# Optimization experiments

Measured on AMD Instinct MI355X. Metric: run time of the kernel, lower is better.

## Reference

```python
import jax, jax.numpy as jnp
import numpy as np

N_NODES = 9
NEG_SLOPE = 0.2
# static edge list from the module (src, dst) pairs, PyG convention row0=src, row1=dst
_E = np.array([[0,1],[1,0],[0,3],[3,0],[0,5],[5,0],[0,7],[7,0],
               [1,2],[2,1],[3,4],[4,3],[5,6],[6,5],[7,8],[8,7]], dtype=np.int32).T
# GATv2Conv default add_self_loops=True
SRC = jnp.asarray(np.concatenate([_E[0], np.arange(N_NODES, dtype=np.int32)]))
DST = jnp.asarray(np.concatenate([_E[1], np.arange(N_NODES, dtype=np.int32)]))


def setup_inputs() -> dict:
    key = jax.random.key(0)
    k1, k2, k3, k4 = jax.random.split(key, 4)
    B, C_IN, C_OUT = 16384, 256, 256
    scale = 1.0 / np.sqrt(C_IN)
    return {
        "x": jax.random.normal(k1, (B, N_NODES, C_IN), jnp.float32),
        "W_l": jax.random.normal(k2, (C_IN, C_OUT), jnp.float32) * scale,
        "W_r": jax.random.normal(k3, (C_IN, C_OUT), jnp.float32) * scale,
        "att": jax.random.normal(k4, (C_OUT,), jnp.float32) * scale,
        "bias": jnp.zeros((C_OUT,), jnp.float32),
    }


def reference(x, W_l, W_r, att, bias):
    # x: [B, N, C_in] batch of identical small graphs
    xl = jnp.einsum("bnc,cd->bnd", x, W_l)  # source-side projection
    xr = jnp.einsum("bnc,cd->bnd", x, W_r)  # target-side projection
    # per-edge GATv2 score: a^T LeakyReLU(x_l[src] + x_r[dst])
    e = jax.nn.leaky_relu(xl[:, SRC] + xr[:, DST], NEG_SLOPE)  # [B, E, C_out]
    score = jnp.einsum("bed,d->be", e, att)                    # [B, E]
    # softmax over incoming edges of each destination node (segment softmax)
    sT = score.T                                               # [E, B]
    m = jax.ops.segment_max(sT, DST, num_segments=N_NODES)     # [N, B]
    ex = jnp.exp(sT - m[DST])
    denom = jax.ops.segment_sum(ex, DST, num_segments=N_NODES)
    alpha = ex / denom[DST]                                    # [E, B]
    # scatter-aggregate messages alpha * x_l[src] into dst
    msg = xl[:, SRC] * alpha.T[..., None]                      # [B, E, C_out]
    out = jax.ops.segment_sum(msg.transpose(1, 0, 2), DST, num_segments=N_NODES)
    return out.transpose(1, 0, 2) + bias                       # [B, N, C_out]
```

## Files before the change

kernel.cpp:

```cpp
#include <hip/hip_runtime.h>
#include <hip/hip_bf16.h>

typedef __attribute__((ext_vector_type(8))) short short8;
typedef __attribute__((ext_vector_type(4))) float f32x4;
typedef __attribute__((ext_vector_type(4))) unsigned short u16x4;

#define STAGE_BYTES (144 * 512)
#define PART_OFF    0
#define ALPHA_OFF   (8 * 25 * 16 * 4)
#define LDS_BYTES   STAGE_BYTES

__device__ __forceinline__ unsigned short f2bf(float f) {
    unsigned int u = __float_as_uint(f);
    unsigned int r = (u + 0x7fffu + ((u >> 16) & 1u)) >> 16;
    return (unsigned short)r;
}

constexpr int C_SRC[25] = {0,1,0,3,0,5,0,7,1,2,3,4,5,6,7,8, 0,1,2,3,4,5,6,7,8};
constexpr int C_DST[25] = {1,0,3,0,5,0,7,0,2,1,4,3,6,5,8,7, 0,1,2,3,4,5,6,7,8};
constexpr int C_NINC[9]  = {5,3,2,3,2,3,2,3,2};
constexpr int C_IOFF[9]  = {0,5,8,10,13,15,18,20,23};
constexpr int C_INCE[25] = {1,3,5,7,16, 0,9,17, 8,18, 2,11,19, 10,20, 4,13,21, 12,22, 6,15,23, 14,24};
constexpr int C_INCS[25] = {1,3,5,7,0,  0,2,1,  1,2,  0,4,3,  3,4,  0,6,5,  5,6,  0,8,7,  7,8};
__device__ const int D_NINC[9]  = {5,3,2,3,2,3,2,3,2};
__device__ const int D_IOFF[9]  = {0,5,8,10,13,15,18,20,23};
__device__ const int D_INCE[25] = {1,3,5,7,16, 0,9,17, 8,18, 2,11,19, 10,20, 4,13,21, 12,22, 6,15,23, 14,24};

__global__ void convert_w_kernel(const float* __restrict__ Wl,
                                 const float* __restrict__ Wr,
                                 unsigned short* __restrict__ WT) {
    int n = blockIdx.x;
    int k = threadIdx.x;
    float v = (n < 256) ? Wl[k * 256 + n] : Wr[k * 256 + (n - 256)];
    WT[n * 256 + k] = f2bf(v);
}

__global__ __launch_bounds__(512, 2) void gat_fused_kernel(
        const float* __restrict__ x,
        const unsigned short* __restrict__ WT,
        const float* __restrict__ att,
        const float* __restrict__ bias,
        float* __restrict__ out) {
    __shared__ __align__(16) char smem[LDS_BYTES];
    float* partials = (float*)(smem + PART_OFF);
    float* alphas   = (float*)(smem + ALPHA_OFF);

    const int tid  = threadIdx.x;
    const int lane = tid & 63;
    const int w    = tid >> 6;
    const int gl   = lane >> 4;
    const int li   = lane & 15;
    const int blk  = blockIdx.x;

    const int c0 = 32 * w + li, c1 = c0 + 16;
    const float attc0 = att[c0], attc1 = att[c1];
    const float bc0   = bias[c0], bc1 = bias[c1];

    const float* xblk = x + (size_t)blk * 36864;
    {
        f32x4 xv[18];
        #pragma unroll
        for (int it = 0; it < 18; ++it)
            xv[it] = *(const f32x4*)(xblk + it * 2048 + tid * 4);
        #pragma unroll
        for (int it = 0; it < 18; ++it) {
            int f    = it * 2048 + tid * 4;
            int gr   = f >> 8;
            int c    = f & 255;
            int g    = gr / 9;
            int node = gr - g * 9;
            int srow = node * 16 + g;
            u16x4 pk = { f2bf(xv[it][0]), f2bf(xv[it][1]), f2bf(xv[it][2]), f2bf(xv[it][3]) };
            *(u16x4*)(smem + srow * 512 + ((2 * c) ^ (g << 4))) = pk;
        }
    }
    __syncthreads();

    const f32x4 ZERO = {0.f, 0.f, 0.f, 0.f};
    f32x4 aL[9][2], aR[9][2];
    #pragma unroll
    for (int m = 0; m < 9; ++m) {
        aL[m][0] = ZERO; aL[m][1] = ZERO; aR[m][0] = ZERO; aR[m][1] = ZERO;
    }
    const unsigned short* WL0 = WT + (size_t)((32 * w + li) * 256 + gl * 8);
    const unsigned short* WL1 = WL0 + 16 * 256;
    const unsigned short* WR0 = WL0 + 256 * 256;
    const unsigned short* WR1 = WR0 + 16 * 256;

    #pragma unroll
    for (int kc = 0; kc < 8; ++kc) {
        short8 bl0 = *(const short8*)(WL0 + kc * 32);
        short8 bl1 = *(const short8*)(WL1 + kc * 32);
        short8 br0 = *(const short8*)(WR0 + kc * 32);
        short8 br1 = *(const short8*)(WR1 + kc * 32);
        const int inner = ((kc * 64) + (gl * 16)) ^ (li << 4);
        short8 am[9];
        #pragma unroll
        for (int m = 0; m < 9; ++m)
            am[m] = *(const short8*)(smem + (m * 16 + li) * 512 + inner);
        #pragma unroll
        for (int m = 0; m < 9; ++m) {
            aL[m][0] = __builtin_amdgcn_mfma_f32_16x16x32_bf16(am[m], bl0, aL[m][0], 0, 0, 0);
            aL[m][1] = __builtin_amdgcn_mfma_f32_16x16x32_bf16(am[m], bl1, aL[m][1], 0, 0, 0);
            aR[m][0] = __builtin_amdgcn_mfma_f32_16x16x32_bf16(am[m], br0, aR[m][0], 0, 0, 0);
            aR[m][1] = __builtin_amdgcn_mfma_f32_16x16x32_bf16(am[m], br1, aR[m][1], 0, 0, 0);
        }
    }
    __syncthreads();

    #pragma unroll
    for (int e = 0; e < 25; ++e) {
        const int s = C_SRC[e], d = C_DST[e];
        float p0 = 0.f, p1 = 0.f, p2 = 0.f, p3 = 0.f;
        #pragma unroll
        for (int nt = 0; nt < 2; ++nt) {
            const float ac = nt ? attc1 : attc0;
            #pragma unroll
            for (int r = 0; r < 4; ++r) {
                float v  = aL[s][nt][r] + aR[d][nt][r];
                float lr = fmaxf(v, 0.2f * v);
                float t  = ac * lr;
                if (r == 0) p0 += t; else if (r == 1) p1 += t;
                else if (r == 2) p2 += t; else p3 += t;
            }
        }
        #pragma unroll
        for (int m = 1; m < 16; m <<= 1) {
            p0 += __shfl_xor(p0, m);
            p1 += __shfl_xor(p1, m);
            p2 += __shfl_xor(p2, m);
            p3 += __shfl_xor(p3, m);
        }
        if (li == 0) {
            f32x4 pk = {p0, p1, p2, p3};
            *(f32x4*)(partials + (w * 25 + e) * 16 + 4 * gl) = pk;
        }
    }
    __syncthreads();

    if (tid < 144) {
        int n = tid >> 4, g = tid & 15;
        int off = D_IOFF[n], cnt = D_NINC[n];
        float mx = -1e30f;
        for (int i = 0; i < cnt; ++i) {
            int e = D_INCE[off + i];
            float s = 0.f;
            #pragma unroll
            for (int ww = 0; ww < 8; ++ww) s += partials[(ww * 25 + e) * 16 + g];
            alphas[e * 16 + g] = s;
            mx = fmaxf(mx, s);
        }
        float ssum = 0.f;
        for (int i = 0; i < cnt; ++i)
            ssum += __expf(alphas[D_INCE[off + i] * 16 + g] - mx);
        float inv = 1.f / ssum;
        for (int i = 0; i < cnt; ++i) {
            int e = D_INCE[off + i];
            alphas[e * 16 + g] = __expf(alphas[e * 16 + g] - mx) * inv;
        }
    }
    __syncthreads();

    #pragma unroll
    for (int n = 0; n < 9; ++n) {
        f32x4 o0 = {bc0, bc0, bc0, bc0};
        f32x4 o1 = {bc1, bc1, bc1, bc1};
        #pragma unroll
        for (int i = 0; i < C_NINC[n]; ++i) {
            const int e  = C_INCE[C_IOFF[n] + i];
            const int sn = C_INCS[C_IOFF[n] + i];
            f32x4 al = *(const f32x4*)(alphas + e * 16 + 4 * gl);
            #pragma unroll
            for (int r = 0; r < 4; ++r) {
                o0[r] += al[r] * aL[sn][0][r];
                o1[r] += al[r] * aL[sn][1][r];
            }
        }
        #pragma unroll
        for (int r = 0; r < 4; ++r) {
            size_t row = (size_t)(blk * 16 + 4 * gl + r) * 9 + n;
            out[row * 256 + c0] = o0[r];
            out[row * 256 + c1] = o1[r];
        }
    }
}

extern "C" void kernel_launch(void* const* d_in, const int* in_sizes, int n_in,
                              void* d_out, int out_size, void* d_ws, size_t ws_size,
                              hipStream_t stream) {
    const float* x    = (const float*)d_in[0];
    const float* Wl   = (const float*)d_in[1];
    const float* Wr   = (const float*)d_in[2];
    const float* att  = (const float*)d_in[3];
    const float* bias = (const float*)d_in[4];
    float* out = (float*)d_out;
    unsigned short* WT = (unsigned short*)d_ws;

    convert_w_kernel<<<512, 256, 0, stream>>>(Wl, Wr, WT);
    gat_fused_kernel<<<1024, 512, 0, stream>>>(x, WT, att, bias, out);
}
```

Before: 140.9 us.

## Split fused GAT block across 16 waves, one 16-column tile per wave

The fused kernel goes from 512 to 1024 threads per block, and each of the 16 waves now owns a single 16-column output tile instead of two. Per-thread accumulator registers drop by half and the staging loads drop from 18 to 9 per thread, aiming for more wavefronts resident per CU and better latency hiding. In exchange, every A fragment is read from LDS twice as often across waves, the cross-wave partial-score reduction doubles to 16 entries, and the launch bound of (1024,4) may force register limits or spills.

Result: slower. 175.9 us (+24.9%).

```diff
diff --git a/kernel.cpp b/kernel.cpp
--- a/kernel.cpp
+++ b/kernel.cpp
@@ -7,7 +7,7 @@
 
 #define STAGE_BYTES (144 * 512)
 #define PART_OFF    0
-#define ALPHA_OFF   (8 * 25 * 16 * 4)
+#define ALPHA_OFF   (16 * 25 * 16 * 4)
 #define LDS_BYTES   STAGE_BYTES
 
 __device__ __forceinline__ unsigned short f2bf(float f) {
@@ -35,7 +35,7 @@
     WT[n * 256 + k] = f2bf(v);
 }
 
-__global__ __launch_bounds__(512, 2) void gat_fused_kernel(
+__global__ __launch_bounds__(1024, 4) void gat_fused_kernel(
         const float* __restrict__ x,
         const unsigned short* __restrict__ WT,
         const float* __restrict__ att,
@@ -52,19 +52,19 @@
     const int li   = lane & 15;
     const int blk  = blockIdx.x;
 
-    const int c0 = 32 * w + li, c1 = c0 + 16;
-    const float attc0 = att[c0], attc1 = att[c1];
-    const float bc0   = bias[c0], bc1 = bias[c1];
+    const int c0 = 16 * w + li;
+    const float attc = att[c0];
+    const float bc   = bias[c0];
 
     const float* xblk = x + (size_t)blk * 36864;
     {
-        f32x4 xv[18];
+        f32x4 xv[9];
         #pragma unroll
-        for (int it = 0; it < 18; ++it)
-            xv[it] = *(const f32x4*)(xblk + it * 2048 + tid * 4);
+        for (int it = 0; it < 9; ++it)
+            xv[it] = *(const f32x4*)(xblk + it * 4096 + tid * 4);
         #pragma unroll
-        for (int it = 0; it < 18; ++it) {
-            int f    = it * 2048 + tid * 4;
+        for (int it = 0; it < 9; ++it) {
+            int f    = it * 4096 + tid * 4;
             int gr   = f >> 8;
             int c    = f & 255;
             int g    = gr / 9;
@@ -77,33 +77,23 @@
     __syncthreads();
 
     const f32x4 ZERO = {0.f, 0.f, 0.f, 0.f};
-    f32x4 aL[9][2], aR[9][2];
+    f32x4 aL[9], aR[9];
     #pragma unroll
-    for (int m = 0; m < 9; ++m) {
-        aL[m][0] = ZERO; aL[m][1] = ZERO; aR[m][0] = ZERO; aR[m][1] = ZERO;
-    }
-    const unsigned short* WL0 = WT + (size_t)((32 * w + li) * 256 + gl * 8);
-    const unsigned short* WL1 = WL0 + 16 * 256;
-    const unsigned short* WR0 = WL0 + 256 * 256;
-    const unsigned short* WR1 = WR0 + 16 * 256;
+    for (int m = 0; m < 9; ++m) { aL[m] = ZERO; aR[m] = ZERO; }
+
+    const unsigned short* WL = WT + (size_t)(c0 * 256 + gl * 8);
+    const unsigned short* WR = WL + 256 * 256;
 
     #pragma unroll
     for (int kc = 0; kc < 8; ++kc) {
-        short8 bl0 = *(const short8*)(WL0 + kc * 32);
-        short8 bl1 = *(const short8*)(WL1 + kc * 32);
-        short8 br0 = *(const short8*)(WR0 + kc * 32);
-        short8 br1 = *(const short8*)(WR1 + kc * 32);
+        short8 bl = *(const short8*)(WL + kc * 32);
+        short8 br = *(const short8*)(WR + kc * 32);
         const int inner = ((kc * 64) + (gl * 16)) ^ (li << 4);
-        short8 am[9];
-        #pragma unroll
-        for (int m = 0; m < 9; ++m)
-            am[m] = *(const short8*)(smem + (m * 16 + li) * 512 + inner);
         #pragma unroll
         for (int m = 0; m < 9; ++m) {
-            aL[m][0] = __builtin_amdgcn_mfma_f32_16x16x32_bf16(am[m], bl0, aL[m][0], 0, 0, 0);
-            aL[m][1] = __builtin_amdgcn_mfma_f32_16x16x32_bf16(am[m], bl1, aL[m][1], 0, 0, 0);
-            aR[m][0] = __builtin_amdgcn_mfma_f32_16x16x32_bf16(am[m], br0, aR[m][0], 0, 0, 0);
-            aR[m][1] = __builtin_amdgcn_mfma_f32_16x16x32_bf16(am[m], br1, aR[m][1], 0, 0, 0);
+            short8 a = *(const short8*)(smem + (m * 16 + li) * 512 + inner);
+            aL[m] = __builtin_amdgcn_mfma_f32_16x16x32_bf16(a, bl, aL[m], 0, 0, 0);
+            aR[m] = __builtin_amdgcn_mfma_f32_16x16x32_bf16(a, br, aR[m], 0, 0, 0);
         }
     }
     __syncthreads();
@@ -111,18 +101,16 @@
     #pragma unroll
     for (int e = 0; e < 25; ++e) {
         const int s = C_SRC[e], d = C_DST[e];
-        float p0 = 0.f, p1 = 0.f, p2 = 0.f, p3 = 0.f;
-        #pragma unroll
-        for (int nt = 0; nt < 2; ++nt) {
-            const float ac = nt ? attc1 : attc0;
-            #pragma unroll
-            for (int r = 0; r < 4; ++r) {
-                float v  = aL[s][nt][r] + aR[d][nt][r];
-                float lr = fmaxf(v, 0.2f * v);
-                float t  = ac * lr;
-                if (r == 0) p0 += t; else if (r == 1) p1 += t;
-                else if (r == 2) p2 += t; else p3 += t;
-            }
+        float p0, p1, p2, p3;
+        {
+            float v0 = aL[s][0] + aR[d][0];
+            float v1 = aL[s][1] + aR[d][1];
+            float v2 = aL[s][2] + aR[d][2];
+            float v3 = aL[s][3] + aR[d][3];
+            p0 = attc * fmaxf(v0, 0.2f * v0);
+            p1 = attc * fmaxf(v1, 0.2f * v1);
+            p2 = attc * fmaxf(v2, 0.2f * v2);
+            p3 = attc * fmaxf(v3, 0.2f * v3);
         }
         #pragma unroll
         for (int m = 1; m < 16; m <<= 1) {
@@ -146,7 +134,7 @@
             int e = D_INCE[off + i];
             float s = 0.f;
             #pragma unroll
-            for (int ww = 0; ww < 8; ++ww) s += partials[(ww * 25 + e) * 16 + g];
+            for (int ww = 0; ww < 16; ++ww) s += partials[(ww * 25 + e) * 16 + g];
             alphas[e * 16 + g] = s;
             mx = fmaxf(mx, s);
         }
@@ -163,24 +151,20 @@
 
     #pragma unroll
     for (int n = 0; n < 9; ++n) {
-        f32x4 o0 = {bc0, bc0, bc0, bc0};
-        f32x4 o1 = {bc1, bc1, bc1, bc1};
+        f32x4 o = {bc, bc, bc, bc};
         #pragma unroll
         for (int i = 0; i < C_NINC[n]; ++i) {
             const int e  = C_INCE[C_IOFF[n] + i];
             const int sn = C_INCS[C_IOFF[n] + i];
             f32x4 al = *(const f32x4*)(alphas + e * 16 + 4 * gl);
             #pragma unroll
-            for (int r = 0; r < 4; ++r) {
-                o0[r] += al[r] * aL[sn][0][r];
-                o1[r] += al[r] * aL[sn][1][r];
-            }
+            for (int r = 0; r < 4; ++r)
+                o[r] += al[r] * aL[sn][r];
         }
         #pragma unroll
         for (int r = 0; r < 4; ++r) {
             size_t row = (size_t)(blk * 16 + 4 * gl + r) * 9 + n;
-            out[row * 256 + c0] = o0[r];
-            out[row * 256 + c1] = o1[r];
+            out[row * 256 + c0] = o[r];
         }
     }
 }
@@ -197,5 +181,5 @@
     unsigned short* WT = (unsigned short*)d_ws;
 
     convert_w_kernel<<<512, 256, 0, stream>>>(Wl, Wr, WT);
-    gat_fused_kernel<<<1024, 512, 0, stream>>>(x, WT, att, bias, out);
+    gat_fused_kernel<<<1024, 1024, 0, stream>>>(x, WT, att, bias, out);
 }
```

## Pack projection accumulators to bf16 and split GEMM phases to raise occupancy

Applied to the files above, without the earlier changes.

The kernel now computes the right projection first and then the left projection in two halves over the node rows. Each finished fp32 accumulator is packed into bf16 pairs, so far fewer registers stay live. The launch bound goes from 2 to 4 blocks per SM, and the x staging loads are split into two batches to cut peak register use. The aim is higher occupancy to hide memory latency. The cost is rounding the xl/xr values to bf16 before the attention scores and the aggregation, which reduces accuracy, plus reloading W and LDS rows across the separate phases.

After: 554.8 us. 3.94x slower.

```diff
diff --git a/kernel.cpp b/kernel.cpp
--- a/kernel.cpp
+++ b/kernel.cpp
@@ -15,6 +15,8 @@
     unsigned int r = (u + 0x7fffu + ((u >> 16) & 1u)) >> 16;
     return (unsigned short)r;
 }
+__device__ __forceinline__ float bflo(unsigned int u) { return __uint_as_float(u << 16); }
+__device__ __forceinline__ float bfhi(unsigned int u) { return __uint_as_float(u & 0xffff0000u); }
 
 constexpr int C_SRC[25] = {0,1,0,3,0,5,0,7,1,2,3,4,5,6,7,8, 0,1,2,3,4,5,6,7,8};
 constexpr int C_DST[25] = {1,0,3,0,5,0,7,0,2,1,4,3,6,5,8,7, 0,1,2,3,4,5,6,7,8};
@@ -35,7 +37,7 @@
     WT[n * 256 + k] = f2bf(v);
 }
 
-__global__ __launch_bounds__(512, 2) void gat_fused_kernel(
+__global__ __launch_bounds__(512, 4) void gat_fused_kernel(
         const float* __restrict__ x,
         const unsigned short* __restrict__ WT,
         const float* __restrict__ att,
@@ -57,14 +59,15 @@
     const float bc0   = bias[c0], bc1 = bias[c1];
 
     const float* xblk = x + (size_t)blk * 36864;
-    {
-        f32x4 xv[18];
-        #pragma unroll
-        for (int it = 0; it < 18; ++it)
-            xv[it] = *(const f32x4*)(xblk + it * 2048 + tid * 4);
-        #pragma unroll
-        for (int it = 0; it < 18; ++it) {
-            int f    = it * 2048 + tid * 4;
+    #pragma unroll
+    for (int b = 0; b < 2; ++b) {
+        f32x4 xv[9];
+        #pragma unroll
+        for (int it = 0; it < 9; ++it)
+            xv[it] = *(const f32x4*)(xblk + (b * 9 + it) * 2048 + tid * 4);
+        #pragma unroll
+        for (int it = 0; it < 9; ++it) {
+            int f    = (b * 9 + it) * 2048 + tid * 4;
             int gr   = f >> 8;
             int c    = f & 255;
             int g    = gr / 9;
@@ -76,34 +79,68 @@
     }
     __syncthreads();
 
+    const unsigned short* WL = WT + (size_t)(c0 * 256 + gl * 8);
+    const unsigned short* WR = WL + 256 * 256;
     const f32x4 ZERO = {0.f, 0.f, 0.f, 0.f};
-    f32x4 aL[9][2], aR[9][2];
-    #pragma unroll
-    for (int m = 0; m < 9; ++m) {
-        aL[m][0] = ZERO; aL[m][1] = ZERO; aR[m][0] = ZERO; aR[m][1] = ZERO;
-    }
-    const unsigned short* WL0 = WT + (size_t)((32 * w + li) * 256 + gl * 8);
-    const unsigned short* WL1 = WL0 + 16 * 256;
-    const unsigned short* WR0 = WL0 + 256 * 256;
-    const unsigned short* WR1 = WR0 + 16 * 256;
-
-    #pragma unroll
-    for (int kc = 0; kc < 8; ++kc) {
-        short8 bl0 = *(const short8*)(WL0 + kc * 32);
-        short8 bl1 = *(const short8*)(WL1 + kc * 32);
-        short8 br0 = *(const short8*)(WR0 + kc * 32);
-        short8 br1 = *(const short8*)(WR1 + kc * 32);
-        const int inner = ((kc * 64) + (gl * 16)) ^ (li << 4);
-        short8 am[9];
+
+    unsigned int aRb[9][2][2];
+    unsigned int aLb[9][2][2];
+
+    {
+        f32x4 aR[9][2];
+        #pragma unroll
+        for (int m = 0; m < 9; ++m) { aR[m][0] = ZERO; aR[m][1] = ZERO; }
+        #pragma unroll
+        for (int kc = 0; kc < 8; ++kc) {
+            short8 br0 = *(const short8*)(WR + kc * 32);
+            short8 br1 = *(const short8*)(WR + 16 * 256 + kc * 32);
+            const int inner = ((kc * 64) + (gl * 16)) ^ (li << 4);
+            #pragma unroll
+            for (int m = 0; m < 9; ++m) {
+                short8 a = *(const short8*)(smem + (m * 16 + li) * 512 + inner);
+                aR[m][0] = __builtin_amdgcn_mfma_f32_16x16x32_bf16(a, br0, aR[m][0], 0, 0, 0);
+                aR[m][1] = __builtin_amdgcn_mfma_f32_16x16x32_bf16(a, br1, aR[m][1], 0, 0, 0);
+            }
+        }
         #pragma unroll
         for (int m = 0; m < 9; ++m)
-            am[m] = *(const short8*)(smem + (m * 16 + li) * 512 + inner);
-        #pragma unroll
-        for (int m = 0; m < 9; ++m) {
-            aL[m][0] = __builtin_amdgcn_mfma_f32_16x16x32_bf16(am[m], bl0, aL[m][0], 0, 0, 0);
-            aL[m][1] = __builtin_amdgcn_mfma_f32_16x16x32_bf16(am[m], bl1, aL[m][1], 0, 0, 0);
-            aR[m][0] = __builtin_amdgcn_mfma_f32_16x16x32_bf16(am[m], br0, aR[m][0], 0, 0, 0);
-            aR[m][1] = __builtin_amdgcn_mfma_f32_16x16x32_bf16(am[m], br1, aR[m][1], 0, 0, 0);
+            #pragma unroll
+            for (int nt = 0; nt < 2; ++nt) {
+                aRb[m][nt][0] = (unsigned int)f2bf(aR[m][nt][0]) | ((unsigned int)f2bf(aR[m][nt][1]) << 16);
+                aRb[m][nt][1] = (unsigned int)f2bf(aR[m][nt][2]) | ((unsigned int)f2bf(aR[m][nt][3]) << 16);
+            }
+    }
+
+    #pragma unroll
+    for (int half = 0; half < 2; ++half) {
+        const int m0 = (half == 0) ? 0 : 5;
+        const int mN = (half == 0) ? 5 : 4;
+        f32x4 aL[5][2];
+        #pragma unroll
+        for (int m = 0; m < 5; ++m) { aL[m][0] = ZERO; aL[m][1] = ZERO; }
+        #pragma unroll
+        for (int kc = 0; kc < 8; ++kc) {
+            short8 bl0 = *(const short8*)(WL + kc * 32);
+            short8 bl1 = *(const short8*)(WL + 16 * 256 + kc * 32);
+            const int inner = ((kc * 64) + (gl * 16)) ^ (li << 4);
+            #pragma unroll
+            for (int m = 0; m < 5; ++m) {
+                if (m < mN) {
+                    short8 a = *(const short8*)(smem + ((m0 + m) * 16 + li) * 512 + inner);
+                    aL[m][0] = __builtin_amdgcn_mfma_f32_16x16x32_bf16(a, bl0, aL[m][0], 0, 0, 0);
+                    aL[m][1] = __builtin_amdgcn_mfma_f32_16x16x32_bf16(a, bl1, aL[m][1], 0, 0, 0);
+                }
+            }
+        }
+        #pragma unroll
+        for (int m = 0; m < 5; ++m) {
+            if (m < mN) {
+                #pragma unroll
+                for (int nt = 0; nt < 2; ++nt) {
+                    aLb[m0 + m][nt][0] = (unsigned int)f2bf(aL[m][nt][0]) | ((unsigned int)f2bf(aL[m][nt][1]) << 16);
+                    aLb[m0 + m][nt][1] = (unsigned int)f2bf(aL[m][nt][2]) | ((unsigned int)f2bf(aL[m][nt][3]) << 16);
+                }
+            }
         }
     }
     __syncthreads();
@@ -115,14 +152,14 @@
         #pragma unroll
         for (int nt = 0; nt < 2; ++nt) {
             const float ac = nt ? attc1 : attc0;
-            #pragma unroll
-            for (int r = 0; r < 4; ++r) {
-                float v  = aL[s][nt][r] + aR[d][nt][r];
-                float lr = fmaxf(v, 0.2f * v);
-                float t  = ac * lr;
-                if (r == 0) p0 += t; else if (r == 1) p1 += t;
-                else if (r == 2) p2 += t; else p3 += t;
-            }
+            float v0 = bflo(aLb[s][nt][0]) + bflo(aRb[d][nt][0]);
+            float v1 = bfhi(aLb[s][nt][0]) + bfhi(aRb[d][nt][0]);
+            float v2 = bflo(aLb[s][nt][1]) + bflo(aRb[d][nt][1]);
+            float v3 = bfhi(aLb[s][nt][1]) + bfhi(aRb[d][nt][1]);
+            p0 += ac * fmaxf(v0, 0.2f * v0);
+            p1 += ac * fmaxf(v1, 0.2f * v1);
+            p2 += ac * fmaxf(v2, 0.2f * v2);
+            p3 += ac * fmaxf(v3, 0.2f * v3);
         }
         #pragma unroll
         for (int m = 1; m < 16; m <<= 1) {
@@ -170,11 +207,14 @@
             const int e  = C_INCE[C_IOFF[n] + i];
             const int sn = C_INCS[C_IOFF[n] + i];
             f32x4 al = *(const f32x4*)(alphas + e * 16 + 4 * gl);
-            #pragma unroll
-            for (int r = 0; r < 4; ++r) {
-                o0[r] += al[r] * aL[sn][0][r];
-                o1[r] += al[r] * aL[sn][1][r];
-            }
+            o0[0] += al[0] * bflo(aLb[sn][0][0]);
+            o0[1] += al[1] * bfhi(aLb[sn][0][0]);
+            o0[2] += al[2] * bflo(aLb[sn][0][1]);
+            o0[3] += al[3] * bfhi(aLb[sn][0][1]);
+            o1[0] += al[0] * bflo(aLb[sn][1][0]);
+            o1[1] += al[1] * bfhi(aLb[sn][1][0]);
+            o1[2] += al[2] * bflo(aLb[sn][1][1]);
+            o1[3] += al[3] * bfhi(aLb[sn][1][1]);
         }
         #pragma unroll
         for (int r = 0; r < 4; ++r) {
```

## Make fused GAT kernel persistent over 4 tiles with double-buffered x staging

Applied to the files above, without the earlier changes.

Each block now processes four 16-graph tiles sequentially, using two LDS stage buffers. The x loads for the next tile are issued during the current tile's epilogue (score reduction, softmax, aggregation), hiding global load latency behind compute. The grid shrinks from 1024 to 256 blocks and LDS use roughly doubles (about 150KB), which limits residency to one 512-thread block per CU and may leave some of the 256 CUs idle. Register pressure also rises from holding prefetched x vectors alongside the accumulators.

Result: slower. 365.7 us (+159.6%).

```diff
diff --git a/kernel.cpp b/kernel.cpp
--- a/kernel.cpp
+++ b/kernel.cpp
@@ -6,9 +6,10 @@
 typedef __attribute__((ext_vector_type(4))) unsigned short u16x4;
 
 #define STAGE_BYTES (144 * 512)
-#define PART_OFF    0
-#define ALPHA_OFF   (8 * 25 * 16 * 4)
-#define LDS_BYTES   STAGE_BYTES
+#define NU 4
+#define PART_OFF  (2 * STAGE_BYTES)
+#define ALPHA_OFF (PART_OFF + 8 * 25 * 16 * 4)
+#define LDS_BYTES (ALPHA_OFF + 25 * 16 * 4)
 
 __device__ __forceinline__ unsigned short f2bf(float f) {
     unsigned int u = __float_as_uint(f);
@@ -50,138 +51,170 @@
     const int w    = tid >> 6;
     const int gl   = lane >> 4;
     const int li   = lane & 15;
-    const int blk  = blockIdx.x;
-
     const int c0 = 32 * w + li, c1 = c0 + 16;
     const float attc0 = att[c0], attc1 = att[c1];
     const float bc0   = bias[c0], bc1 = bias[c1];
 
-    const float* xblk = x + (size_t)blk * 36864;
-    {
-        f32x4 xv[18];
-        #pragma unroll
-        for (int it = 0; it < 18; ++it)
-            xv[it] = *(const f32x4*)(xblk + it * 2048 + tid * 4);
-        #pragma unroll
-        for (int it = 0; it < 18; ++it) {
-            int f    = it * 2048 + tid * 4;
+    auto stage_batch = [&](char* dst, const f32x4* xv, int b) {
+        #pragma unroll
+        for (int it = 0; it < 9; ++it) {
+            int f    = (b * 9 + it) * 2048 + tid * 4;
             int gr   = f >> 8;
             int c    = f & 255;
             int g    = gr / 9;
             int node = gr - g * 9;
             int srow = node * 16 + g;
             u16x4 pk = { f2bf(xv[it][0]), f2bf(xv[it][1]), f2bf(xv[it][2]), f2bf(xv[it][3]) };
-            *(u16x4*)(smem + srow * 512 + ((2 * c) ^ (g << 4))) = pk;
+            *(u16x4*)(dst + srow * 512 + ((2 * c) ^ (g << 4))) = pk;
+        }
+    };
+
+    const unsigned short* WL = WT + (size_t)(c0 * 256 + gl * 8);
+    const unsigned short* WR = WL + 256 * 256;
+    const f32x4 ZERO = {0.f, 0.f, 0.f, 0.f};
+
+    {
+        const float* xblk = x + (size_t)(blockIdx.x * NU) * 36864;
+        #pragma unroll
+        for (int b = 0; b < 2; ++b) {
+            f32x4 xv[9];
+            #pragma unroll
+            for (int it = 0; it < 9; ++it)
+                xv[it] = *(const f32x4*)(xblk + (b * 9 + it) * 2048 + tid * 4);
+            stage_batch(smem, xv, b);
         }
     }
     __syncthreads();
 
-    const f32x4 ZERO = {0.f, 0.f, 0.f, 0.f};
-    f32x4 aL[9][2], aR[9][2];
-    #pragma unroll
-    for (int m = 0; m < 9; ++m) {
-        aL[m][0] = ZERO; aL[m][1] = ZERO; aR[m][0] = ZERO; aR[m][1] = ZERO;
-    }
-    const unsigned short* WL0 = WT + (size_t)((32 * w + li) * 256 + gl * 8);
-    const unsigned short* WL1 = WL0 + 16 * 256;
-    const unsigned short* WR0 = WL0 + 256 * 256;
-    const unsigned short* WR1 = WR0 + 16 * 256;
-
-    #pragma unroll
-    for (int kc = 0; kc < 8; ++kc) {
-        short8 bl0 = *(const short8*)(WL0 + kc * 32);
-        short8 bl1 = *(const short8*)(WL1 + kc * 32);
-        short8 br0 = *(const short8*)(WR0 + kc * 32);
-        short8 br1 = *(const short8*)(WR1 + kc * 32);
-        const int inner = ((kc * 64) + (gl * 16)) ^ (li << 4);
-        short8 am[9];
-        #pragma unroll
-        for (int m = 0; m < 9; ++m)
-            am[m] = *(const short8*)(smem + (m * 16 + li) * 512 + inner);
+    int cur = 0;
+    for (int u = 0; u < NU; ++u) {
+        char* bufc = smem + cur * STAGE_BYTES;
+        char* bufn = smem + (cur ^ 1) * STAGE_BYTES;
+        const bool more = (u + 1 < NU);
+        const float* xnext = x + (size_t)(blockIdx.x * NU + u + 1) * 36864;
+
+        f32x4 aL[9][2], aR[9][2];
         #pragma unroll
         for (int m = 0; m < 9; ++m) {
-            aL[m][0] = __builtin_amdgcn_mfma_f32_16x16x32_bf16(am[m], bl0, aL[m][0], 0, 0, 0);
-            aL[m][1] = __builtin_amdgcn_mfma_f32_16x16x32_bf16(am[m], bl1, aL[m][1], 0, 0, 0);
-            aR[m][0] = __builtin_amdgcn_mfma_f32_16x16x32_bf16(am[m], br0, aR[m][0], 0, 0, 0);
-            aR[m][1] = __builtin_amdgcn_mfma_f32_16x16x32_bf16(am[m], br1, aR[m][1], 0, 0, 0);
-        }
-    }
-    __syncthreads();
-
-    #pragma unroll
-    for (int e = 0; e < 25; ++e) {
-        const int s = C_SRC[e], d = C_DST[e];
-        float p0 = 0.f, p1 = 0.f, p2 = 0.f, p3 = 0.f;
-        #pragma unroll
-        for (int nt = 0; nt < 2; ++nt) {
-            const float ac = nt ? attc1 : attc0;
+            aL[m][0] = ZERO; aL[m][1] = ZERO; aR[m][0] = ZERO; aR[m][1] = ZERO;
+        }
+        #pragma unroll
+        for (int kc = 0; kc < 8; ++kc) {
+            short8 bl0 = *(const short8*)(WL + kc * 32);
+            short8 bl1 = *(const short8*)(WL + 16 * 256 + kc * 32);
+            short8 br0 = *(const short8*)(WR + kc * 32);
+            short8 br1 = *(const short8*)(WR + 16 * 256 + kc * 32);
+            const int inner = ((kc * 64) + (gl * 16)) ^ (li << 4);
+            short8 am[9];
+            #pragma unroll
+            for (int m = 0; m < 9; ++m)
+                am[m] = *(const short8*)(bufc + (m * 16 + li) * 512 + inner);
+            #pragma unroll
+            for (int m = 0; m < 9; ++m) {
+                aL[m][0] = __builtin_amdgcn_mfma_f32_16x16x32_bf16(am[m], bl0, aL[m][0], 0, 0, 0);
+                aL[m][1] = __builtin_amdgcn_mfma_f32_16x16x32_bf16(am[m], bl1, aL[m][1], 0, 0, 0);
+                aR[m][0] = __builtin_amdgcn_mfma_f32_16x16x32_bf16(am[m], br0, aR[m][0], 0, 0, 0);
+                aR[m][1] = __builtin_amdgcn_mfma_f32_16x16x32_bf16(am[m], br1, aR[m][1], 0, 0, 0);
+            }
+        }
+
+        f32x4 xv0[9];
+        if (more) {
+            #pragma unroll
+            for (int it = 0; it < 9; ++it)
+                xv0[it] = *(const f32x4*)(xnext + it * 2048 + tid * 4);
+        }
+        __builtin_amdgcn_sched_barrier(0);
+
+        #pragma unroll
+        for (int e = 0; e < 25; ++e) {
+            const int s = C_SRC[e], d = C_DST[e];
+            float p0 = 0.f, p1 = 0.f, p2 = 0.f, p3 = 0.f;
+            #pragma unroll
+            for (int nt = 0; nt < 2; ++nt) {
+                const float ac = nt ? attc1 : attc0;
+                #pragma unroll
+                for (int r = 0; r < 4; ++r) {
+                    float v  = aL[s][nt][r] + aR[d][nt][r];
+                    float lr = fmaxf(v, 0.2f * v);
+                    float t  = ac * lr;
+                    if (r == 0) p0 += t; else if (r == 1) p1 += t;
+                    else if (r == 2) p2 += t; else p3 += t;
+                }
+            }
+            #pragma unroll
+            for (int m = 1; m < 16; m <<= 1) {
+                p0 += __shfl_xor(p0, m);
+                p1 += __shfl_xor(p1, m);
+                p2 += __shfl_xor(p2, m);
+                p3 += __shfl_xor(p3, m);
+            }
+            if (li == 0) {
+                f32x4 pk = {p0, p1, p2, p3};
+                *(f32x4*)(partials + (w * 25 + e) * 16 + 4 * gl) = pk;
+            }
+        }
+        __syncthreads();
+
+        f32x4 xv1[9];
+        if (more) {
+            stage_batch(bufn, xv0, 0);
+            #pragma unroll
+            for (int it = 0; it < 9; ++it)
+                xv1[it] = *(const f32x4*)(xnext + (9 + it) * 2048 + tid * 4);
+        }
+        __builtin_amdgcn_sched_barrier(0);
+
+        if (tid < 144) {
+            int n = tid >> 4, g = tid & 15;
+            int off = D_IOFF[n], cnt = D_NINC[n];
+            float mx = -1e30f;
+            for (int i = 0; i < cnt; ++i) {
+                int e = D_INCE[off + i];
+                float s = 0.f;
+                #pragma unroll
+                for (int ww = 0; ww < 8; ++ww) s += partials[(ww * 25 + e) * 16 + g];
+                alphas[e * 16 + g] = s;
+                mx = fmaxf(mx, s);
+            }
+            float ssum = 0.f;
+            for (int i = 0; i < cnt; ++i)
+                ssum += __expf(alphas[D_INCE[off + i] * 16 + g] - mx);
+            float inv = 1.f / ssum;
+            for (int i = 0; i < cnt; ++i) {
+                int e = D_INCE[off + i];
+                alphas[e * 16 + g] = __expf(alphas[e * 16 + g] - mx) * inv;
+            }
+        }
+        __syncthreads();
+
+        if (more) stage_batch(bufn, xv1, 1);
+
+        float* outblk = out + (size_t)(blockIdx.x * NU + u) * 36864;
+        #pragma unroll
+        for (int n = 0; n < 9; ++n) {
+            f32x4 o0 = {bc0, bc0, bc0, bc0};
+            f32x4 o1 = {bc1, bc1, bc1, bc1};
+            #pragma unroll
+            for (int i = 0; i < C_NINC[n]; ++i) {
+                const int e  = C_INCE[C_IOFF[n] + i];
+                const int sn = C_INCS[C_IOFF[n] + i];
+                f32x4 al = *(const f32x4*)(alphas + e * 16 + 4 * gl);
+                #pragma unroll
+                for (int r = 0; r < 4; ++r) {
+                    o0[r] += al[r] * aL[sn][0][r];
+                    o1[r] += al[r] * aL[sn][1][r];
+                }
+            }
             #pragma unroll
             for (int r = 0; r < 4; ++r) {
-                float v  = aL[s][nt][r] + aR[d][nt][r];
-                float lr = fmaxf(v, 0.2f * v);
-                float t  = ac * lr;
-                if (r == 0) p0 += t; else if (r == 1) p1 += t;
-                else if (r == 2) p2 += t; else p3 += t;
-            }
-        }
-        #pragma unroll
-        for (int m = 1; m < 16; m <<= 1) {
-            p0 += __shfl_xor(p0, m);
-            p1 += __shfl_xor(p1, m);
-            p2 += __shfl_xor(p2, m);
-            p3 += __shfl_xor(p3, m);
-        }
-        if (li == 0) {
-            f32x4 pk = {p0, p1, p2, p3};
-            *(f32x4*)(partials + (w * 25 + e) * 16 + 4 * gl) = pk;
-        }
-    }
-    __syncthreads();
-
-    if (tid < 144) {
-        int n = tid >> 4, g = tid & 15;
-        int off = D_IOFF[n], cnt = D_NINC[n];
-        float mx = -1e30f;
-        for (int i = 0; i < cnt; ++i) {
-            int e = D_INCE[off + i];
-            float s = 0.f;
-            #pragma unroll
-            for (int ww = 0; ww < 8; ++ww) s += partials[(ww * 25 + e) * 16 + g];
-            alphas[e * 16 + g] = s;
-            mx = fmaxf(mx, s);
-        }
-        float ssum = 0.f;
-        for (int i = 0; i < cnt; ++i)
-            ssum += __expf(alphas[D_INCE[off + i] * 16 + g] - mx);
-        float inv = 1.f / ssum;
-        for (int i = 0; i < cnt; ++i) {
-            int e = D_INCE[off + i];
-            alphas[e * 16 + g] = __expf(alphas[e * 16 + g] - mx) * inv;
-        }
-    }
-    __syncthreads();
-
-    #pragma unroll
-    for (int n = 0; n < 9; ++n) {
-        f32x4 o0 = {bc0, bc0, bc0, bc0};
-        f32x4 o1 = {bc1, bc1, bc1, bc1};
-        #pragma unroll
-        for (int i = 0; i < C_NINC[n]; ++i) {
-            const int e  = C_INCE[C_IOFF[n] + i];
-            const int sn = C_INCS[C_IOFF[n] + i];
-            f32x4 al = *(const f32x4*)(alphas + e * 16 + 4 * gl);
-            #pragma unroll
-            for (int r = 0; r < 4; ++r) {
-                o0[r] += al[r] * aL[sn][0][r];
-                o1[r] += al[r] * aL[sn][1][r];
-            }
-        }
-        #pragma unroll
-        for (int r = 0; r < 4; ++r) {
-            size_t row = (size_t)(blk * 16 + 4 * gl + r) * 9 + n;
-            out[row * 256 + c0] = o0[r];
-            out[row * 256 + c1] = o1[r];
-        }
+                int row = (4 * gl + r) * 9 + n;
+                outblk[row * 256 + c0] = o0[r];
+                outblk[row * 256 + c1] = o1[r];
+            }
+        }
+        __syncthreads();
+        cur ^= 1;
     }
 }
 
@@ -197,5 +230,5 @@
     unsigned short* WT = (unsigned short*)d_ws;
 
     convert_w_kernel<<<512, 256, 0, stream>>>(Wl, Wr, WT);
-    gat_fused_kernel<<<1024, 512, 0, stream>>>(x, WT, att, bias, out);
-}
+    gat_fused_kernel<<<256, 512, 0, stream>>>(x, WT, att, bias, out);
+}
```
